# Kernel optimization log

Hardware: AMD Instinct MI355X
Metric: run time of the kernel (lower is better)

Reference implementation:

```python
import jax, jax.numpy as jnp
import numpy as np

NUM_HEADS = 16
HEAD_DIM = 64  # hidden_size 1024 / 16 heads


def setup_inputs() -> dict:
    key = jax.random.key(0)
    k1, k2 = jax.random.split(key)
    B, S, D = 2, 2048, 1024
    hidden_states = jax.random.normal(k1, (B, S, D), dtype=jnp.float32)
    # fast_qkv: bias-free fused qkv projection + separate q/v biases (init zeros in torch)
    W_qkv = jax.random.normal(k2, (D, 3 * D), dtype=jnp.float32) * (1.0 / np.sqrt(D))
    q_bias = jnp.zeros((D,), dtype=jnp.float32)
    v_bias = jnp.zeros((D,), dtype=jnp.float32)
    return {"hidden_states": hidden_states, "W_qkv": W_qkv, "q_bias": q_bias, "v_bias": v_bias}


def reference(hidden_states, W_qkv, q_bias, v_bias):
    B, S, D = hidden_states.shape
    H, hd = NUM_HEADS, HEAD_DIM
    qkv = hidden_states @ W_qkv                      # (B,S,3D)
    q, k, v = jnp.split(qkv, 3, axis=-1)
    q = q + q_bias
    v = v + v_bias
    # (B,S,H,hd)
    q = q.reshape(B, S, H, hd)
    k = k.reshape(B, S, H, hd)
    v = v.reshape(B, S, H, hd)
    q = q / jnp.sqrt(jnp.asarray(hd, dtype=q.dtype))
    # full (B,H,S,S) score tensor, softmax in fp32 then cast back (matches torch)
    scores = jnp.einsum('bqhd,bkhd->bhqk', q, k)
    probs = jax.nn.softmax(scores.astype(jnp.float32), axis=-1).astype(v.dtype)
    ctx = jnp.einsum('bhqk,bkhd->bqhd', probs, v)    # (B,S,H,hd)
    return ctx.reshape(B, S, D)
```

## Files before the change

### kernel.cpp

```cpp
#include <hip/hip_runtime.h>
#include <hip/hip_bf16.h>

typedef _Float16 half_t;
typedef _Float16 h8 __attribute__((ext_vector_type(8)));
typedef _Float16 h4 __attribute__((ext_vector_type(4)));
typedef _Float16 h2 __attribute__((ext_vector_type(2)));
typedef float f32x4 __attribute__((ext_vector_type(4)));
typedef float f4 __attribute__((ext_vector_type(4)));

#define DEVI __device__ __forceinline__

constexpr int NB = 2;
constexpr int S  = 2048;
constexpr int DM = 1024;
constexpr int NH = 16;
constexpr int HD = 64;
constexpr long M = (long)NB * S;
constexpr int N3 = 3 * DM;

DEVI f32x4 mfma16(h8 a, h8 b, f32x4 c) {
  return __builtin_amdgcn_mfma_f32_16x16x32_f16(a, b, c, 0, 0, 0);
}
DEVI f32x4 mfma16h(h4 a, h4 b, f32x4 c) {
  return __builtin_amdgcn_mfma_f32_16x16x16f16(a, b, c, 0, 0, 0);
}
DEVI h8 ld8h(const half_t* p) { return *(const h8*)p; }

#if __has_builtin(__builtin_amdgcn_exp2f)
DEVI float ex2(float x) { return __builtin_amdgcn_exp2f(x); }
#else
DEVI float ex2(float x) { float r; asm("v_exp_f32 %0, %1" : "=v"(r) : "v"(x)); return r; }
#endif

DEVI h2 pk2(float a, float b) {
  auto r = __builtin_amdgcn_cvt_pkrtz(a, b);
  h2 o; __builtin_memcpy(&o, &r, sizeof(o)); return o;
}

DEVI void gl_lds16(const half_t* g, half_t* l) {
  __builtin_amdgcn_global_load_lds(
      (const __attribute__((address_space(1))) void*)g,
      (__attribute__((address_space(3))) void*)l, 16, 0, 0);
}

__global__ void prep(const float* __restrict__ hidden, half_t* __restrict__ Hb,
                     const float* __restrict__ W, half_t* __restrict__ Wt) {
  __shared__ float tile[32][33];
  const int id = blockIdx.x, t = threadIdx.x;
  if (id < 2048) {
    const long i = ((long)id * 256 + t) * 8;
    const f4 a = *(const f4*)(hidden + i), b = *(const f4*)(hidden + i + 4);
    h8 r;
    #pragma unroll
    for (int k = 0; k < 4; k++) { r[k] = (half_t)a[k]; r[4 + k] = (half_t)b[k]; }
    *(h8*)(Hb + i) = r;
  } else {
    const int id2 = id - 2048;
    const int c0 = (id2 % 96) * 32, r0 = (id2 / 96) * 32;
    const int x = t & 31, y = t >> 5;
    #pragma unroll
    for (int i = 0; i < 32; i += 8) tile[y + i][x] = W[(long)(r0 + y + i) * N3 + c0 + x];
    __syncthreads();
    #pragma unroll
    for (int i = 0; i < 32; i += 8)
      Wt[(long)(c0 + y + i) * DM + r0 + x] = (half_t)tile[x][y + i];
  }
}

__global__ __launch_bounds__(256) void qkv_gemm(
    const half_t* __restrict__ A, const half_t* __restrict__ Bt,
    const float* __restrict__ qbias, const float* __restrict__ vbias,
    half_t* __restrict__ Qf, half_t* __restrict__ Kf, half_t* __restrict__ Vt)
{
  constexpr int BM = 128, BN = 128, BK = 32;
  __shared__ alignas(16) half_t As[3][BM * BK];
  __shared__ alignas(16) half_t Bs[3][BN * BK];
  const int t = threadIdx.x, lane = t & 63, wave = t >> 6;
  const int quad = lane >> 4, l16 = lane & 15;
  const int id = blockIdx.x, xcd = id & 7, jj = id >> 3;
  const int m0 = (xcd * 4 + (jj & 3)) * BM;
  const int n0 = (jj >> 2) * BN;
  const int wm = (wave & 1) * 64, wn = (wave >> 1) * 64;

  const half_t* aP0 = A  + (long)(m0 + (t >> 2)) * DM + (t & 3) * 8;
  const half_t* aP1 = aP0 + (long)64 * DM;
  const half_t* bP0 = Bt + (long)(n0 + (t >> 2)) * DM + (t & 3) * 8;
  const half_t* bP1 = bP0 + (long)64 * DM;
  const int wb = wave * 512;

  f32x4 acc[4][4] = {};

  {
    gl_lds16(aP0, &As[0][wb]);
    gl_lds16(aP1, &As[0][wb] + 2048);
    gl_lds16(bP0, &Bs[0][wb]);
    gl_lds16(bP1, &Bs[0][wb] + 2048);
    gl_lds16(aP0 + BK, &As[1][wb]);
    gl_lds16(aP1 + BK, &As[1][wb] + 2048);
    gl_lds16(bP0 + BK, &Bs[1][wb]);
    gl_lds16(bP1 + BK, &Bs[1][wb] + 2048);
    asm volatile("s_waitcnt vmcnt(4)" ::: "memory");
    __builtin_amdgcn_sched_barrier(0);
    __builtin_amdgcn_s_barrier();
  }

  constexpr int NKT = DM / BK;
  for (int kt = 0; kt < NKT; ++kt) {
    const int cur = kt % 3;
    if (kt + 2 < NKT) {
      const int nsl = (kt + 2) % 3, k0 = (kt + 2) * BK;
      gl_lds16(aP0 + k0, &As[nsl][wb]);
      gl_lds16(aP1 + k0, &As[nsl][wb] + 2048);
      gl_lds16(bP0 + k0, &Bs[nsl][wb]);
      gl_lds16(bP1 + k0, &Bs[nsl][wb] + 2048);
    }

    h8 af[4], bfr[4];
    #pragma unroll
    for (int i = 0; i < 4; i++) af[i]  = ld8h(&As[cur][(wm + i * 16 + l16) * BK + quad * 8]);
    #pragma unroll
    for (int j = 0; j < 4; j++) bfr[j] = ld8h(&Bs[cur][(wn + j * 16 + l16) * BK + quad * 8]);
    #pragma unroll
    for (int i = 0; i < 4; i++)
      #pragma unroll
      for (int j = 0; j < 4; j++)
        acc[i][j] = mfma16(af[i], bfr[j], acc[i][j]);

    if (kt + 1 < NKT) {
      if (kt + 2 < NKT) asm volatile("s_waitcnt vmcnt(4)" ::: "memory");
      else              asm volatile("s_waitcnt vmcnt(0)" ::: "memory");
      __builtin_amdgcn_sched_barrier(0);
      __builtin_amdgcn_s_barrier();
    }
  }

  if (n0 < 2 * DM) {
    #pragma unroll
    for (int i = 0; i < 4; i++) {
      #pragma unroll
      for (int j = 0; j < 4; j++) {
        const int n = n0 + wn + j * 16 + l16;
        #pragma unroll
        for (int r = 0; r < 4; r++) {
          const long m = m0 + wm + i * 16 + quad * 4 + r;
          const float cv = acc[i][j][r];
          if (n < DM) {
            Qf[m * DM + n] = (half_t)((cv + qbias[n]) * 0.1803368801f);
          } else {
            Kf[m * DM + (n - DM)] = (half_t)cv;
          }
        }
      }
    }
  } else {
    const int dBase = n0 + wn - 2 * DM;
    #pragma unroll
    for (int i = 0; i < 4; i++) {
      const long mb = m0 + wm + i * 16 + quad * 4;
      const int bb = (int)(mb >> 11);
      const int ss = (int)(mb & (S - 1));
      #pragma unroll
      for (int j = 0; j < 4; j++) {
        const int dd = dBase + j * 16 + l16;
        const float vb4 = vbias[dd];
        h4 vv;
        #pragma unroll
        for (int r = 0; r < 4; r++) vv[r] = (half_t)(acc[i][j][r] + vb4);
        *(h4*)&Vt[(((long)bb * NH + (dd >> 6)) * HD + (dd & 63)) * S + ss] = vv;
      }
    }
  }
}

__global__ __launch_bounds__(512) void attn(
    const half_t* __restrict__ Qf, const half_t* __restrict__ Kf,
    const half_t* __restrict__ Vt, float* __restrict__ out)
{
  constexpr int LK = 72, LV = 72;
  __shared__ alignas(16) half_t smem[2 * 64 * LK + 2 * 64 * LV];
  half_t* const KsB = smem;
  half_t* const VsB = smem + 2 * 64 * LK;

  const int bh = blockIdx.y, b = bh >> 4, h = bh & 15;
  const int qt = blockIdx.x;
  const int t = threadIdx.x, lane = t & 63, wave = t >> 6;
  const int w4 = wave & 3, kvh = wave >> 2;
  const int quad = lane >> 4, l16 = lane & 15;

  const long qrow0 = (long)b * S + qt * 128 + w4 * 32;
  const half_t* qg = Qf + qrow0 * DM + h * HD;
  const long kb0 = (long)kvh * (S / 2);
  const half_t* kg = Kf + ((long)b * S + kb0) * DM + h * HD;
  const half_t* vg = Vt + (long)bh * HD * S + kb0;

  h8 bq[2][2];
  #pragma unroll
  for (int qi = 0; qi < 2; qi++)
    #pragma unroll
    for (int dh = 0; dh < 2; dh++)
      bq[qi][dh] = ld8h(&qg[(long)(qi * 16 + l16) * DM + dh * 32 + quad * 8]);

  const int tg = t & 255;
  const int r0s = tg >> 3, c0s = (tg & 7) * 8;
  const int r1s = 32 + r0s;
  half_t* const ksW = KsB + kvh * (64 * LK);
  half_t* const vsW = VsB + kvh * (64 * LV);
  h8 kreg[2], vreg[2];
  kreg[0] = ld8h(&kg[(long)r0s * DM + c0s]);
  kreg[1] = ld8h(&kg[(long)r1s * DM + c0s]);
  vreg[0] = ld8h(&vg[(long)r0s * S + c0s]);
  vreg[1] = ld8h(&vg[(long)r1s * S + c0s]);

  const f32x4 z4 = {0.f, 0.f, 0.f, 0.f};
  const h4 vones = {(half_t)1.f, (half_t)1.f, (half_t)1.f, (half_t)1.f};

  f32x4 O[2][4] = {};
  f32x4 lacc[2] = {};

  constexpr int NT = (S / 2) / 64;
  for (int kt = 0; kt < NT; ++kt) {
    __syncthreads();
    *(h8*)&ksW[r0s * LK + c0s] = kreg[0];
    *(h8*)&ksW[r1s * LK + c0s] = kreg[1];
    *(h8*)&vsW[r0s * LV + c0s] = vreg[0];
    *(h8*)&vsW[r1s * LV + c0s] = vreg[1];
    __syncthreads();

    if (kt < NT - 1) {
      const long ko = (long)(kt + 1) * 64;
      kreg[0] = ld8h(&kg[(ko + r0s) * DM + c0s]);
      kreg[1] = ld8h(&kg[(ko + r1s) * DM + c0s]);
      vreg[0] = ld8h(&vg[(long)r0s * S + ko + c0s]);
      vreg[1] = ld8h(&vg[(long)r1s * S + ko + c0s]);
    }

    h4 pa[2][4];
    #pragma unroll
    for (int g = 0; g < 4; g++) {
      const h8 kf0 = ld8h(&ksW[(g * 16 + l16) * LK + quad * 8]);
      const h8 kf1 = ld8h(&ksW[(g * 16 + l16) * LK + 32 + quad * 8]);
      #pragma unroll
      for (int qi = 0; qi < 2; qi++) {
        f32x4 sc = mfma16(kf0, bq[qi][0], z4);
        sc = mfma16(kf1, bq[qi][1], sc);
        const h2 lo = pk2(ex2(sc[0]), ex2(sc[1]));
        const h2 hi = pk2(ex2(sc[2]), ex2(sc[3]));
        union { h4 v; h2 p[2]; } u; u.p[0] = lo; u.p[1] = hi;
        pa[qi][g] = u.v;
      }
    }

    #pragma unroll
    for (int g = 0; g < 4; g++) {
      lacc[0] = mfma16h(pa[0][g], vones, lacc[0]);
      lacc[1] = mfma16h(pa[1][g], vones, lacc[1]);
    }

    #pragma unroll
    for (int j = 0; j < 4; j++) {
      #pragma unroll
      for (int g = 0; g < 4; g++) {
        const h4 vf = *(const h4*)&vsW[(j * 16 + l16) * LV + g * 16 + quad * 4];
        O[0][j] = mfma16h(pa[0][g], vf, O[0][j]);
        O[1][j] = mfma16h(pa[1][g], vf, O[1][j]);
      }
    }
  }

  __syncthreads();
  float* const xb = (float*)smem;
  float* const xl = xb + 8192;
  if (kvh) {
    #pragma unroll
    for (int qi = 0; qi < 2; qi++) {
      #pragma unroll
      for (int j = 0; j < 4; j++)
        *(f4*)&xb[(((w4 * 2 + qi) * 4 + j) * 64 + lane) * 4] = O[qi][j];
      if (l16 == 0) {
        #pragma unroll
        for (int r = 0; r < 4; r++)
          xl[(w4 * 2 + qi) * 16 + quad * 4 + r] = lacc[qi][r];
      }
    }
  }
  __syncthreads();
  if (!kvh) {
    #pragma unroll
    for (int qi = 0; qi < 2; qi++) {
      #pragma unroll
      for (int j = 0; j < 4; j++)
        O[qi][j] += *(const f4*)&xb[(((w4 * 2 + qi) * 4 + j) * 64 + lane) * 4];
      #pragma unroll
      for (int r = 0; r < 4; r++) {
        const float linv = 1.f / (lacc[qi][r] + xl[(w4 * 2 + qi) * 16 + quad * 4 + r]);
        const long srow = qrow0 + qi * 16 + quad * 4 + r;
        #pragma unroll
        for (int j = 0; j < 4; j++)
          out[srow * DM + h * HD + j * 16 + l16] = O[qi][j][r] * linv;
      }
    }
  }
}

extern "C" void kernel_launch(void* const* d_in, const int* in_sizes, int n_in,
                              void* d_out, int out_size, void* d_ws, size_t ws_size,
                              hipStream_t stream) {
  (void)in_sizes; (void)n_in; (void)out_size; (void)ws_size;
  const float* hidden = (const float*)d_in[0];
  const float* W      = (const float*)d_in[1];
  const float* qbias  = (const float*)d_in[2];
  const float* vbias  = (const float*)d_in[3];
  float* out = (float*)d_out;

  half_t* ws = (half_t*)d_ws;
  half_t* Hb = ws;
  half_t* Wt = Hb + M * DM;
  half_t* Qf = Wt + (long)N3 * DM;
  half_t* Kf = Qf + M * DM;
  half_t* Vt = Kf + M * DM;

  prep<<<2048 + 3072, 256, 0, stream>>>(hidden, Hb, W, Wt);
  qkv_gemm<<<(N3 / 128) * (int)(M / 128), 256, 0, stream>>>(Hb, Wt, qbias, vbias, Qf, Kf, Vt);
  attn<<<dim3(S / 128, NB * NH), 512, 0, stream>>>(Qf, Kf, Vt, out);
}
```

Before: 176.3 us.

## Permute V tile layout in LDS for 16-byte reads and remap blocks per XCD

```diff
diff --git a/kernel.cpp b/kernel.cpp
--- a/kernel.cpp
+++ b/kernel.cpp
@@ -42,6 +42,8 @@
       (const __attribute__((address_space(1))) void*)g,
       (__attribute__((address_space(3))) void*)l, 16, 0, 0);
 }
+
+union H8U { h8 v; h4 q[2]; };
 
 __global__ void prep(const float* __restrict__ hidden, half_t* __restrict__ Hb,
                      const float* __restrict__ W, half_t* __restrict__ Wt) {
@@ -181,8 +183,10 @@
   half_t* const KsB = smem;
   half_t* const VsB = smem + 2 * 64 * LK;
 
-  const int bh = blockIdx.y, b = bh >> 4, h = bh & 15;
-  const int qt = blockIdx.x;
+  const int id = blockIdx.x;
+  const int xcd = id & 7, slot = id >> 3;
+  const int bh = xcd * 4 + (slot >> 4), qt = slot & 15;
+  const int b = bh >> 4, h = bh & 15;
   const int t = threadIdx.x, lane = t & 63, wave = t >> 6;
   const int w4 = wave & 3, kvh = wave >> 2;
   const int quad = lane >> 4, l16 = lane & 15;
@@ -203,13 +207,15 @@
   const int tg = t & 255;
   const int r0s = tg >> 3, c0s = (tg & 7) * 8;
   const int r1s = 32 + r0s;
+  const int a = tg & 7;
+  const int vb0 = ((a & 1) << 5) | ((a >> 1) << 2);
   half_t* const ksW = KsB + kvh * (64 * LK);
   half_t* const vsW = VsB + kvh * (64 * LV);
-  h8 kreg[2], vreg[2];
-  kreg[0] = ld8h(&kg[(long)r0s * DM + c0s]);
-  kreg[1] = ld8h(&kg[(long)r1s * DM + c0s]);
-  vreg[0] = ld8h(&vg[(long)r0s * S + c0s]);
-  vreg[1] = ld8h(&vg[(long)r1s * S + c0s]);
+  h8 kreg[2]; H8U vreg[2];
+  kreg[0]   = ld8h(&kg[(long)r0s * DM + c0s]);
+  kreg[1]   = ld8h(&kg[(long)r1s * DM + c0s]);
+  vreg[0].v = ld8h(&vg[(long)r0s * S + c0s]);
+  vreg[1].v = ld8h(&vg[(long)r1s * S + c0s]);
 
   const f32x4 z4 = {0.f, 0.f, 0.f, 0.f};
   const h4 vones = {(half_t)1.f, (half_t)1.f, (half_t)1.f, (half_t)1.f};
@@ -222,16 +228,18 @@
     __syncthreads();
     *(h8*)&ksW[r0s * LK + c0s] = kreg[0];
     *(h8*)&ksW[r1s * LK + c0s] = kreg[1];
-    *(h8*)&vsW[r0s * LV + c0s] = vreg[0];
-    *(h8*)&vsW[r1s * LV + c0s] = vreg[1];
+    *(h4*)&vsW[r0s * LV + vb0]      = vreg[0].q[0];
+    *(h4*)&vsW[r0s * LV + vb0 + 16] = vreg[0].q[1];
+    *(h4*)&vsW[r1s * LV + vb0]      = vreg[1].q[0];
+    *(h4*)&vsW[r1s * LV + vb0 + 16] = vreg[1].q[1];
     __syncthreads();
 
     if (kt < NT - 1) {
       const long ko = (long)(kt + 1) * 64;
-      kreg[0] = ld8h(&kg[(ko + r0s) * DM + c0s]);
-      kreg[1] = ld8h(&kg[(ko + r1s) * DM + c0s]);
-      vreg[0] = ld8h(&vg[(long)r0s * S + ko + c0s]);
-      vreg[1] = ld8h(&vg[(long)r1s * S + ko + c0s]);
+      kreg[0]   = ld8h(&kg[(ko + r0s) * DM + c0s]);
+      kreg[1]   = ld8h(&kg[(ko + r1s) * DM + c0s]);
+      vreg[0].v = ld8h(&vg[(long)r0s * S + ko + c0s]);
+      vreg[1].v = ld8h(&vg[(long)r1s * S + ko + c0s]);
     }
 
     h4 pa[2][4];
@@ -258,12 +266,17 @@
 
     #pragma unroll
     for (int j = 0; j < 4; j++) {
-      #pragma unroll
-      for (int g = 0; g < 4; g++) {
-        const h4 vf = *(const h4*)&vsW[(j * 16 + l16) * LV + g * 16 + quad * 4];
-        O[0][j] = mfma16h(pa[0][g], vf, O[0][j]);
-        O[1][j] = mfma16h(pa[1][g], vf, O[1][j]);
-      }
+      H8U v01, v23;
+      v01.v = ld8h(&vsW[(j * 16 + l16) * LV + quad * 16]);
+      v23.v = ld8h(&vsW[(j * 16 + l16) * LV + quad * 16 + 8]);
+      O[0][j] = mfma16h(pa[0][0], v01.q[0], O[0][j]);
+      O[1][j] = mfma16h(pa[1][0], v01.q[0], O[1][j]);
+      O[0][j] = mfma16h(pa[0][1], v01.q[1], O[0][j]);
+      O[1][j] = mfma16h(pa[1][1], v01.q[1], O[1][j]);
+      O[0][j] = mfma16h(pa[0][2], v23.q[0], O[0][j]);
+      O[1][j] = mfma16h(pa[1][2], v23.q[0], O[1][j]);
+      O[0][j] = mfma16h(pa[0][3], v23.q[1], O[0][j]);
+      O[1][j] = mfma16h(pa[1][3], v23.q[1], O[1][j]);
     }
   }
 
@@ -321,5 +334,5 @@
 
   prep<<<2048 + 3072, 256, 0, stream>>>(hidden, Hb, W, Wt);
   qkv_gemm<<<(N3 / 128) * (int)(M / 128), 256, 0, stream>>>(Hb, Wt, qbias, vbias, Qf, Kf, Vt);
-  attn<<<dim3(S / 128, NB * NH), 512, 0, stream>>>(Qf, Kf, Vt, out);
-}
+  attn<<<512, 512, 0, stream>>>(Qf, Kf, Vt, out);
+}
```

Result: faster. 172.6 us, median of 2 (-2.1%).
